# Optimization experiments

Hardware: AMD Instinct MI355X
Metric: run time of the kernel (lower is better)

## Reference

```python
import jax, jax.numpy as jnp
import numpy as np

N = 50000   # nodes
H = 4       # heads
R = 3       # relations
E = 524288  # edges per relation


def _gatv2_rel(x, Wsrc, Wdst, a, src, dst, n_heads):
    """Single-relation GATv2: returns [N, H, D] aggregated messages."""
    hs = (x @ Wsrc).reshape(x.shape[0], n_heads, -1)  # [N,H,D]
    hd = (x @ Wdst).reshape(x.shape[0], n_heads, -1)  # [N,H,D]
    m = hs[src] + hd[dst]                              # [E,H,D] gather
    e = jnp.einsum('ehd,hd->eh', jax.nn.leaky_relu(m, 0.2), a)  # [E,H]
    # segment softmax over incoming edges of each destination node
    emax = jax.ops.segment_max(e, dst, num_segments=N)          # [N,H]
    ee = jnp.exp(e - emax[dst])
    den = jax.ops.segment_sum(ee, dst, num_segments=N)          # [N,H]
    alpha = ee / (den[dst] + 1e-9)                              # [E,H]
    msg = alpha[..., None] * hs[src]                            # [E,H,D]
    return jax.ops.segment_sum(msg, dst, num_segments=N)        # [N,H,D]


def setup_inputs() -> dict:
    key = jax.random.key(0)
    ks = jax.random.split(key, 9)
    sc = lambda f: 1.0 / np.sqrt(f)
    return {
        'x': jax.random.normal(ks[0], (N, 128), jnp.float32),
        'src': jax.random.randint(ks[1], (R, E), 0, N, jnp.int32),
        'dst': jax.random.randint(ks[2], (R, E), 0, N, jnp.int32),
        'W1_src': jax.random.normal(ks[3], (R, 128, 128), jnp.float32) * sc(128),
        'W1_dst': jax.random.normal(ks[4], (R, 128, 128), jnp.float32) * sc(128),
        'a1': jax.random.normal(ks[5], (R, H, 32), jnp.float32) * sc(32),
        'W2_src': jax.random.normal(ks[6], (R, 128, 256), jnp.float32) * sc(128),
        'W2_dst': jax.random.normal(ks[7], (R, 128, 256), jnp.float32) * sc(128),
        'a2': jax.random.normal(ks[8], (R, H, 64), jnp.float32) * sc(64),
    }


def reference(x, src, dst, W1_src, W1_dst, a1, W2_src, W2_dst, a2):
    # Layer 1: sum GATv2 over relations, relu, flatten heads -> [N, hid]
    h = jnp.zeros((N, H, 32), x.dtype)
    for r in range(R):
        h = h + _gatv2_rel(x, W1_src[r], W1_dst[r], a1[r], src[r], dst[r], H)
    h = jax.nn.relu(h).reshape(N, H * 32)  # [N, 128]
    # Layer 2: sum GATv2 over relations -> [N, H, out]
    out = jnp.zeros((N, H, 64), x.dtype)
    for r in range(R):
        out = out + _gatv2_rel(h, W2_src[r], W2_dst[r], a2[r], src[r], dst[r], H)
    return out
```

## Files before the change

### kernel.cpp

```cpp
#include <hip/hip_runtime.h>
#include <hip/hip_bf16.h>

#define NN 50000
#define HH 4
#define RR 3
#define EE 524288
#define ESHIFT 19
#define TN (RR*NN)
#define NCHUNK ((TN + 1023)/1024)
#define LOG2E 1.4426950408889634f

typedef __attribute__((ext_vector_type(8))) short short8;
typedef __attribute__((ext_vector_type(4))) short short4v;
typedef __attribute__((ext_vector_type(4))) float float4v;
typedef __attribute__((ext_vector_type(2))) float float2v;
typedef __attribute__((ext_vector_type(2))) _Float16 half2v;

#if defined(__has_builtin)
#if __has_builtin(__builtin_amdgcn_fdot2)
#define USE_FDOT2 1
#else
#define USE_FDOT2 0
#endif
#else
#define USE_FDOT2 0
#endif


__global__ void conv_bf16x4_kernel(const float* __restrict__ in, short4v* __restrict__ out) {
    int i = blockIdx.x * 256 + threadIdx.x;
    float4v v = ((const float4v*)in)[i];
    short4v o;
    o.x = (short)__bfloat16_as_ushort(__float2bfloat16(v.x));
    o.y = (short)__bfloat16_as_ushort(__float2bfloat16(v.y));
    o.z = (short)__bfloat16_as_ushort(__float2bfloat16(v.z));
    o.w = (short)__bfloat16_as_ushort(__float2bfloat16(v.w));
    out[i] = o;
}

__global__ void transpose_w_kernel(const float* __restrict__ W, __hip_bfloat16* __restrict__ T,
                                   int NC, int colOff) {
    int i = blockIdx.x * 256 + threadIdx.x;
    int per = 128 * NC;
    int r = i / per;
    int rem = i - r * per;
    int k = rem / NC;
    int n = rem - k * NC;
    T[(size_t)(r * 2 * NC + colOff + n) * 128 + k] = __float2bfloat16(W[i]);
}


__global__ void hist_kernel(const int* __restrict__ dst, int* __restrict__ deg) {
    int i = blockIdx.x * 256 + threadIdx.x;
    int r = i >> ESHIFT;
    atomicAdd(&deg[r * NN + dst[i]], 1);
}

__global__ void scan1_kernel(const int* __restrict__ deg, int* __restrict__ part) {
    __shared__ int s[256];
    int t = threadIdx.x;
    int base = blockIdx.x * 1024 + t * 4;
    int sum = 0;
#pragma unroll
    for (int j = 0; j < 4; j++) {
        int idx = base + j;
        sum += (idx < TN) ? deg[idx] : 0;
    }
    s[t] = sum;
    __syncthreads();
    for (int off = 128; off > 0; off >>= 1) {
        if (t < off) s[t] += s[t + off];
        __syncthreads();
    }
    if (t == 0) part[blockIdx.x] = s[0];
}

__global__ void scan2_kernel(int* part) {
    int run = 0;
    for (int i = 0; i < NCHUNK; i++) {
        int v = part[i];
        part[i] = run;
        run += v;
    }
}

__global__ void scan3_kernel(const int* __restrict__ deg, const int* __restrict__ part,
                             int* __restrict__ offs, int* __restrict__ curs) {
    __shared__ int s[256];
    int t = threadIdx.x;
    int base = blockIdx.x * 1024 + t * 4;
    int v[4];
    int tsum = 0;
#pragma unroll
    for (int j = 0; j < 4; j++) {
        int idx = base + j;
        v[j] = (idx < TN) ? deg[idx] : 0;
        tsum += v[j];
    }
    s[t] = tsum;
    __syncthreads();
    for (int off = 1; off < 256; off <<= 1) {
        int x = (t >= off) ? s[t - off] : 0;
        __syncthreads();
        s[t] += x;
        __syncthreads();
    }
    int excl = s[t] - tsum + part[blockIdx.x];
    int run = excl;
#pragma unroll
    for (int j = 0; j < 4; j++) {
        int idx = base + j;
        if (idx < TN) {
            offs[idx] = run;
            curs[idx] = run;
            run += v[j];
        }
    }
}

__global__ void scatter_kernel(const int* __restrict__ src, const int* __restrict__ dst,
                               int* __restrict__ curs, int* __restrict__ esrc) {
    int i = blockIdx.x * 256 + threadIdx.x;
    int p = blockIdx.y;
    int d = dst[i];
    if ((unsigned)(d - p * 12500) < 12500u) {
        int r = i >> ESHIFT;
        int pos = atomicAdd(&curs[r * NN + d], 1);
        esrc[pos] = src[i] << 8;
    }
}


__launch_bounds__(256)
__global__ void gemm_kernel(const __hip_bfloat16* __restrict__ A,
                            const __hip_bfloat16* __restrict__ Bt,
                            _Float16* __restrict__ C,
                            int M, int nshift, int tilesPerSplit) {
    __shared__ __hip_bfloat16 Bs[64 * 136];
    int tile_m = blockIdx.x * 64;
    int t = threadIdx.x;
    int w = t >> 6, lane = t & 63;
    int m16 = lane & 15, quad = lane >> 4;
    int row = tile_m + w * 16 + m16;
    int rowc = row < M ? row : M - 1;

    short8 a[4];
    const short8* ap = (const short8*)(A + (size_t)rowc * 128);
#pragma unroll
    for (int kf = 0; kf < 4; kf++) a[kf] = ap[quad + kf * 4];

    int cmask = (1 << nshift) - 1;
    int tn0 = blockIdx.y * tilesPerSplit;
    int tn1 = tn0 + tilesPerSplit;

    for (int tn = tn0; tn < tn1; ++tn) {
        int tile_n = tn * 64;
        {
            const uint4* gsrc = (const uint4*)(Bt + (size_t)tile_n * 128);
#pragma unroll
            for (int e = t; e < 64 * 16; e += 256) {
                int n = e >> 4, c = e & 15;
                uint4 val = gsrc[n * 16 + c];
                *(uint4*)(&Bs[n * 136 + c * 8]) = val;
            }
        }
        __syncthreads();

        float4v acc[4];
#pragma unroll
        for (int ct = 0; ct < 4; ct++) {
            acc[ct] = (float4v){0.f, 0.f, 0.f, 0.f};
            const short8* bp = (const short8*)(Bs + (ct * 16 + m16) * 136);
#pragma unroll
            for (int kf = 0; kf < 4; kf++) {
                short8 b = bp[quad + kf * 4];
                acc[ct] = __builtin_amdgcn_mfma_f32_16x16x32_bf16(a[kf], b, acc[ct], 0, 0, 0);
            }
        }
        __syncthreads();

#pragma unroll
        for (int ct = 0; ct < 4; ct++) {
            int col = tile_n + ct * 16 + m16;
            int tbl = col >> nshift;
            int cc = col & cmask;
            size_t base = ((size_t)tbl * M) << nshift;
#pragma unroll
            for (int rg = 0; rg < 4; rg++) {
                int rr = tile_m + w * 16 + quad * 4 + rg;
                if (rr < M) C[base + (((size_t)rr) << nshift) + cc] = (_Float16)acc[ct][rg];
            }
        }
    }
}


template <int W2>
__device__ inline void ldrow16(const char* __restrict__ p, half2v* hv) {
    if constexpr (W2 == 2) {
        uint2 pk = *(const uint2*)p;
        hv[0] = __builtin_bit_cast(half2v, pk.x);
        hv[1] = __builtin_bit_cast(half2v, pk.y);
    } else {
        uint4 pk = *(const uint4*)p;
        hv[0] = __builtin_bit_cast(half2v, pk.x);
        hv[1] = __builtin_bit_cast(half2v, pk.y);
        hv[2] = __builtin_bit_cast(half2v, pk.z);
        hv[3] = __builtin_bit_cast(half2v, pk.w);
    }
}

template <int W2>
__device__ inline float edot16(const half2v* hv, const half2v* hdv, const half2v* al) {
    const half2v c02 = {(_Float16)0.2f, (_Float16)0.2f};
    float s = 0.f;
#pragma unroll
    for (int j = 0; j < W2; j++) {
        half2v m = hv[j] + hdv[j];
        half2v lr = __builtin_elementwise_max(m, m * c02);
#if USE_FDOT2
        s = __builtin_amdgcn_fdot2(lr, al[j], s, false);
#else
        half2v tt = lr * al[j];
        s += (float)tt.x + (float)tt.y;
#endif
    }
    return s;
}

template <int CTRL>
__device__ inline float dpp_add(float s) {
    int t = __builtin_amdgcn_update_dpp(0, __float_as_int(s), CTRL, 0xF, 0xF, true);
    return s + __int_as_float(t);
}

__device__ inline float hred8(float s) {
    s = dpp_add<0xB1>(s);
    s = dpp_add<0x4E>(s);
    s = dpp_add<0x141>(s);
    return s;
}

template <int W2, bool L1, int SH>
__launch_bounds__(256)
__global__ void agg_kernel(const char* __restrict__ C,
                           const float* __restrict__ a,
                           const int* __restrict__ offs, const int* __restrict__ deg,
                           const int* __restrict__ esrc,
                           float* __restrict__ outf, __hip_bfloat16* __restrict__ outb) {
    const int V = 2 * W2;
    const int NC = 32 * V;
    const int ROWB = NC * 2;
    int wid = (blockIdx.x * 256 + threadIdx.x) >> 6;
    int lane = threadIdx.x & 63;
    int g = lane >> 5;
    int c = lane & 31;
    int eb = c * V;
    int ebb = eb * 2;

    float2v total[W2];
#pragma unroll
    for (int j = 0; j < W2; j++) total[j] = (float2v){0.f, 0.f};

#pragma unroll 1
    for (int r = 0; r < RR; r++) {
        const char* hsb = C + (size_t)(2 * r) * NN * ROWB + ebb;
        const char* hdb = C + (size_t)(2 * r + 1) * NN * ROWB + ebb;
        half2v hdv[W2], al[W2];
        float2v acc[W2];
        ldrow16<W2>(hdb + (size_t)wid * ROWB, hdv);
#pragma unroll
        for (int j = 0; j < W2; j++) {
            al[j] = (half2v){(_Float16)(a[r * NC + eb + 2 * j] * LOG2E),
                             (_Float16)(a[r * NC + eb + 2 * j + 1] * LOG2E)};
            acc[j] = (float2v){0.f, 0.f};
        }
        float den = 0.f;
        int e0 = offs[r * NN + wid];
        int dg = deg[r * NN + wid];
        int elast = e0 + dg - 1;
        int nit = (dg + 7) >> 3;
        int kbase = (g << 2);
        int u0 = esrc[min(e0 + kbase,     elast)];
        int u1 = esrc[min(e0 + kbase + 1, elast)];
        int u2 = esrc[min(e0 + kbase + 2, elast)];
        int u3 = esrc[min(e0 + kbase + 3, elast)];
        for (int it = 0; it < nit; ++it) {
            int k = (it << 3) + kbase;
            int kn = k + 8;
            int n0 = esrc[min(e0 + kn,     elast)];
            int n1 = esrc[min(e0 + kn + 1, elast)];
            int n2 = esrc[min(e0 + kn + 2, elast)];
            int n3 = esrc[min(e0 + kn + 3, elast)];
            half2v hv0[W2], hv1[W2], hv2[W2], hv3[W2];
            ldrow16<W2>(hsb + ((size_t)(unsigned)u0 << SH), hv0);
            ldrow16<W2>(hsb + ((size_t)(unsigned)u1 << SH), hv1);
            ldrow16<W2>(hsb + ((size_t)(unsigned)u2 << SH), hv2);
            ldrow16<W2>(hsb + ((size_t)(unsigned)u3 << SH), hv3);
            float s0 = hred8(edot16<W2>(hv0, hdv, al));
            float s1 = hred8(edot16<W2>(hv1, hdv, al));
            float s2 = hred8(edot16<W2>(hv2, hdv, al));
            float s3 = hred8(edot16<W2>(hv3, hdv, al));
            float p0 = (k     < dg) ? __builtin_amdgcn_exp2f(s0) : 0.f;
            float p1 = (k + 1 < dg) ? __builtin_amdgcn_exp2f(s1) : 0.f;
            float p2 = (k + 2 < dg) ? __builtin_amdgcn_exp2f(s2) : 0.f;
            float p3 = (k + 3 < dg) ? __builtin_amdgcn_exp2f(s3) : 0.f;
            den += (p0 + p1) + (p2 + p3);
#pragma unroll
            for (int j = 0; j < W2; j++) {
                acc[j].x = __builtin_fmaf(p0, (float)hv0[j].x, acc[j].x);
                acc[j].y = __builtin_fmaf(p0, (float)hv0[j].y, acc[j].y);
                acc[j].x = __builtin_fmaf(p1, (float)hv1[j].x, acc[j].x);
                acc[j].y = __builtin_fmaf(p1, (float)hv1[j].y, acc[j].y);
                acc[j].x = __builtin_fmaf(p2, (float)hv2[j].x, acc[j].x);
                acc[j].y = __builtin_fmaf(p2, (float)hv2[j].y, acc[j].y);
                acc[j].x = __builtin_fmaf(p3, (float)hv3[j].x, acc[j].x);
                acc[j].y = __builtin_fmaf(p3, (float)hv3[j].y, acc[j].y);
            }
            u0 = n0; u1 = n1; u2 = n2; u3 = n3;
        }
        den += __shfl_xor(den, 32);
        float inv = 1.f / (den + 1e-9f);
        float2v iv = (float2v){inv, inv};
#pragma unroll
        for (int j = 0; j < W2; j++) {
            float2v tt = acc[j];
            tt.x += __shfl_xor(tt.x, 32);
            tt.y += __shfl_xor(tt.y, 32);
            total[j] += tt * iv;
        }
    }

    if (g == 0) {
        if constexpr (L1) {
#pragma unroll
            for (int j = 0; j < W2; j++) {
                float v0 = total[j].x, v1 = total[j].y;
                outb[(size_t)wid * NC + eb + 2 * j]     = __float2bfloat16(v0 > 0.f ? v0 : 0.f);
                outb[(size_t)wid * NC + eb + 2 * j + 1] = __float2bfloat16(v1 > 0.f ? v1 : 0.f);
            }
        } else {
#pragma unroll
            for (int j = 0; j < W2; j++) {
                outf[(size_t)wid * NC + eb + 2 * j]     = total[j].x;
                outf[(size_t)wid * NC + eb + 2 * j + 1] = total[j].y;
            }
        }
    }
}


extern "C" void kernel_launch(void* const* d_in, const int* in_sizes, int n_in,
                              void* d_out, int out_size, void* d_ws, size_t ws_size,
                              hipStream_t stream) {
    const float* x   = (const float*)d_in[0];
    const int*   src = (const int*)d_in[1];
    const int*   dst = (const int*)d_in[2];
    const float* W1s = (const float*)d_in[3];
    const float* W1d = (const float*)d_in[4];
    const float* a1  = (const float*)d_in[5];
    const float* W2s = (const float*)d_in[6];
    const float* W2d = (const float*)d_in[7];
    const float* a2  = (const float*)d_in[8];

    char* ws = (char*)d_ws;
    size_t off = 0;
    auto alloc = [&](size_t bytes) -> void* {
        void* p = ws + off;
        off += (bytes + 255) & ~(size_t)255;
        return p;
    };
    __hip_bfloat16* xb = (__hip_bfloat16*)alloc((size_t)NN * 128 * 2);
    __hip_bfloat16* hb = (__hip_bfloat16*)alloc((size_t)NN * 128 * 2);
    _Float16*       Cb = (_Float16*)alloc((size_t)NN * 1536 * 2);
    __hip_bfloat16* T1 = (__hip_bfloat16*)alloc((size_t)768 * 128 * 2);
    __hip_bfloat16* T2 = (__hip_bfloat16*)alloc((size_t)1536 * 128 * 2);
    int* deg  = (int*)alloc((size_t)TN * 4);
    int* offs = (int*)alloc((size_t)TN * 4);
    int* curs = (int*)alloc((size_t)TN * 4);
    int* esrc = (int*)alloc((size_t)RR * EE * 4);
    int* part = (int*)alloc(4096);

    float* outp = (float*)d_out;

    conv_bf16x4_kernel<<<6250, 256, 0, stream>>>(x, (short4v*)xb);
    transpose_w_kernel<<<192, 256, 0, stream>>>(W1s, T1, 128, 0);
    transpose_w_kernel<<<192, 256, 0, stream>>>(W1d, T1, 128, 128);
    transpose_w_kernel<<<384, 256, 0, stream>>>(W2s, T2, 256, 0);
    transpose_w_kernel<<<384, 256, 0, stream>>>(W2d, T2, 256, 256);

    hipMemsetAsync(deg, 0, (size_t)TN * 4, stream);
    hist_kernel<<<(RR * EE) / 256, 256, 0, stream>>>(dst, deg);
    scan1_kernel<<<NCHUNK, 256, 0, stream>>>(deg, part);
    scan2_kernel<<<1, 1, 0, stream>>>(part);
    scan3_kernel<<<NCHUNK, 256, 0, stream>>>(deg, part, offs, curs);
    scatter_kernel<<<dim3((RR * EE) / 256, 4), 256, 0, stream>>>(src, dst, curs, esrc);

    gemm_kernel<<<dim3(782, 3), 256, 0, stream>>>(xb, T1, Cb, NN, 7, 4);
    agg_kernel<2, true, 0><<<12500, 256, 0, stream>>>((const char*)Cb, a1, offs, deg, esrc,
                                                      nullptr, hb);

    gemm_kernel<<<dim3(782, 4), 256, 0, stream>>>(hb, T2, Cb, NN, 8, 6);
    agg_kernel<4, false, 1><<<12500, 256, 0, stream>>>((const char*)Cb, a2, offs, deg, esrc,
                                                       outp, nullptr);
}
```

Before: 570.1 us.

## Software-pipeline source row gathers and hoist per-relation setup loads in aggregation kernel

Source feature rows for the next group of edges are now loaded while the current group is being computed, a double-buffered register pipeline with index prefetch two iterations ahead. All per-relation offsets, degrees, first source indices, destination rows and attention vectors are loaded up front, and the relation loop is fully unrolled. The goal is to hide gather latency in the edge loop. The cost is much higher register pressure, which may reduce occupancy, and it issues extra speculative loads past the end of each node's edge list. Zero-degree nodes are clamped so those loads stay in range.

```diff
diff --git a/kernel.cpp b/kernel.cpp
--- a/kernel.cpp
+++ b/kernel.cpp
@@ -257,50 +257,80 @@
     int c = lane & 31;
     int eb = c * V;
     int ebb = eb * 2;
+    int kbase = g << 2;
+
+    int e0v[RR], dgv[RR], elastv[RR];
+#pragma unroll
+    for (int r = 0; r < RR; r++) {
+        e0v[r] = offs[r * NN + wid];
+        dgv[r] = deg[r * NN + wid];
+    }
+#pragma unroll
+    for (int r = 0; r < RR; r++)
+        elastv[r] = e0v[r] + ((dgv[r] > 0) ? dgv[r] : 1) - 1;
+
+    int u[RR][4];
+#pragma unroll
+    for (int r = 0; r < RR; r++)
+#pragma unroll
+        for (int q = 0; q < 4; q++)
+            u[r][q] = esrc[min(e0v[r] + kbase + q, elastv[r])];
+
+    half2v hdv[RR][W2];
+#pragma unroll
+    for (int r = 0; r < RR; r++) {
+        const char* hdb = C + (size_t)(2 * r + 1) * NN * ROWB + ebb;
+        ldrow16<W2>(hdb + (size_t)wid * ROWB, hdv[r]);
+    }
+
+    half2v al[RR][W2];
+#pragma unroll
+    for (int r = 0; r < RR; r++)
+#pragma unroll
+        for (int j = 0; j < W2; j++)
+            al[r][j] = (half2v){(_Float16)(a[r * NC + eb + 2 * j] * LOG2E),
+                                (_Float16)(a[r * NC + eb + 2 * j + 1] * LOG2E)};
 
     float2v total[W2];
 #pragma unroll
     for (int j = 0; j < W2; j++) total[j] = (float2v){0.f, 0.f};
 
-#pragma unroll 1
+#pragma unroll
     for (int r = 0; r < RR; r++) {
         const char* hsb = C + (size_t)(2 * r) * NN * ROWB + ebb;
-        const char* hdb = C + (size_t)(2 * r + 1) * NN * ROWB + ebb;
-        half2v hdv[W2], al[W2];
+        int e0 = e0v[r], dg = dgv[r], elast = elastv[r];
+        int nit = (dg + 7) >> 3;
+        float den = 0.f;
         float2v acc[W2];
-        ldrow16<W2>(hdb + (size_t)wid * ROWB, hdv);
-#pragma unroll
-        for (int j = 0; j < W2; j++) {
-            al[j] = (half2v){(_Float16)(a[r * NC + eb + 2 * j] * LOG2E),
-                             (_Float16)(a[r * NC + eb + 2 * j + 1] * LOG2E)};
-            acc[j] = (float2v){0.f, 0.f};
-        }
-        float den = 0.f;
-        int e0 = offs[r * NN + wid];
-        int dg = deg[r * NN + wid];
-        int elast = e0 + dg - 1;
-        int nit = (dg + 7) >> 3;
-        int kbase = (g << 2);
-        int u0 = esrc[min(e0 + kbase,     elast)];
-        int u1 = esrc[min(e0 + kbase + 1, elast)];
-        int u2 = esrc[min(e0 + kbase + 2, elast)];
-        int u3 = esrc[min(e0 + kbase + 3, elast)];
+#pragma unroll
+        for (int j = 0; j < W2; j++) acc[j] = (float2v){0.f, 0.f};
+
+        half2v hA0[W2], hA1[W2], hA2[W2], hA3[W2];
+        ldrow16<W2>(hsb + ((size_t)(unsigned)u[r][0] << SH), hA0);
+        ldrow16<W2>(hsb + ((size_t)(unsigned)u[r][1] << SH), hA1);
+        ldrow16<W2>(hsb + ((size_t)(unsigned)u[r][2] << SH), hA2);
+        ldrow16<W2>(hsb + ((size_t)(unsigned)u[r][3] << SH), hA3);
+        int n0 = esrc[min(e0 + kbase + 8,  elast)];
+        int n1 = esrc[min(e0 + kbase + 9,  elast)];
+        int n2 = esrc[min(e0 + kbase + 10, elast)];
+        int n3 = esrc[min(e0 + kbase + 11, elast)];
+
         for (int it = 0; it < nit; ++it) {
             int k = (it << 3) + kbase;
-            int kn = k + 8;
-            int n0 = esrc[min(e0 + kn,     elast)];
-            int n1 = esrc[min(e0 + kn + 1, elast)];
-            int n2 = esrc[min(e0 + kn + 2, elast)];
-            int n3 = esrc[min(e0 + kn + 3, elast)];
-            half2v hv0[W2], hv1[W2], hv2[W2], hv3[W2];
-            ldrow16<W2>(hsb + ((size_t)(unsigned)u0 << SH), hv0);
-            ldrow16<W2>(hsb + ((size_t)(unsigned)u1 << SH), hv1);
-            ldrow16<W2>(hsb + ((size_t)(unsigned)u2 << SH), hv2);
-            ldrow16<W2>(hsb + ((size_t)(unsigned)u3 << SH), hv3);
-            float s0 = hred8(edot16<W2>(hv0, hdv, al));
-            float s1 = hred8(edot16<W2>(hv1, hdv, al));
-            float s2 = hred8(edot16<W2>(hv2, hdv, al));
-            float s3 = hred8(edot16<W2>(hv3, hdv, al));
+            half2v hB0[W2], hB1[W2], hB2[W2], hB3[W2];
+            ldrow16<W2>(hsb + ((size_t)(unsigned)n0 << SH), hB0);
+            ldrow16<W2>(hsb + ((size_t)(unsigned)n1 << SH), hB1);
+            ldrow16<W2>(hsb + ((size_t)(unsigned)n2 << SH), hB2);
+            ldrow16<W2>(hsb + ((size_t)(unsigned)n3 << SH), hB3);
+            int kn = k + 16;
+            int m0 = esrc[min(e0 + kn,     elast)];
+            int m1 = esrc[min(e0 + kn + 1, elast)];
+            int m2 = esrc[min(e0 + kn + 2, elast)];
+            int m3 = esrc[min(e0 + kn + 3, elast)];
+            float s0 = hred8(edot16<W2>(hA0, hdv[r], al[r]));
+            float s1 = hred8(edot16<W2>(hA1, hdv[r], al[r]));
+            float s2 = hred8(edot16<W2>(hA2, hdv[r], al[r]));
+            float s3 = hred8(edot16<W2>(hA3, hdv[r], al[r]));
             float p0 = (k     < dg) ? __builtin_amdgcn_exp2f(s0) : 0.f;
             float p1 = (k + 1 < dg) ? __builtin_amdgcn_exp2f(s1) : 0.f;
             float p2 = (k + 2 < dg) ? __builtin_amdgcn_exp2f(s2) : 0.f;
@@ -308,16 +338,20 @@
             den += (p0 + p1) + (p2 + p3);
 #pragma unroll
             for (int j = 0; j < W2; j++) {
-                acc[j].x = __builtin_fmaf(p0, (float)hv0[j].x, acc[j].x);
-                acc[j].y = __builtin_fmaf(p0, (float)hv0[j].y, acc[j].y);
-                acc[j].x = __builtin_fmaf(p1, (float)hv1[j].x, acc[j].x);
-                acc[j].y = __builtin_fmaf(p1, (float)hv1[j].y, acc[j].y);
-                acc[j].x = __builtin_fmaf(p2, (float)hv2[j].x, acc[j].x);
-                acc[j].y = __builtin_fmaf(p2, (float)hv2[j].y, acc[j].y);
-                acc[j].x = __builtin_fmaf(p3, (float)hv3[j].x, acc[j].x);
-                acc[j].y = __builtin_fmaf(p3, (float)hv3[j].y, acc[j].y);
-            }
-            u0 = n0; u1 = n1; u2 = n2; u3 = n3;
+                acc[j].x = __builtin_fmaf(p0, (float)hA0[j].x, acc[j].x);
+                acc[j].y = __builtin_fmaf(p0, (float)hA0[j].y, acc[j].y);
+                acc[j].x = __builtin_fmaf(p1, (float)hA1[j].x, acc[j].x);
+                acc[j].y = __builtin_fmaf(p1, (float)hA1[j].y, acc[j].y);
+                acc[j].x = __builtin_fmaf(p2, (float)hA2[j].x, acc[j].x);
+                acc[j].y = __builtin_fmaf(p2, (float)hA2[j].y, acc[j].y);
+                acc[j].x = __builtin_fmaf(p3, (float)hA3[j].x, acc[j].x);
+                acc[j].y = __builtin_fmaf(p3, (float)hA3[j].y, acc[j].y);
+            }
+#pragma unroll
+            for (int j = 0; j < W2; j++) {
+                hA0[j] = hB0[j]; hA1[j] = hB1[j]; hA2[j] = hB2[j]; hA3[j] = hB3[j];
+            }
+            n0 = m0; n1 = m1; n2 = m2; n3 = m3;
         }
         den += __shfl_xor(den, 32);
         float inv = 1.f / (den + 1e-9f);
```

Result: slower. 585.6 us (+2.7%).
